# Kernel tuning notes

Measured on AMD Instinct MI355X. Metric: run time of the kernel, lower is better.

## Reference

```python
import jax, jax.numpy as jnp
import numpy as np

D = 64; T = 128; B = 64; R = 20; SEE = 10; H = 4; C = 4
N = 300000; P = 4000; K = 256


def setup_inputs() -> dict:
    key = jax.random.key(0)
    ks = jax.random.split(key, 24)
    g = lambda k, s: jax.random.normal(k, s, dtype=jnp.float32) * 0.05
    return {
        "prob_id": jax.random.randint(ks[0], (T, B), 0, P),
        "skills": jax.random.randint(ks[1], (T, B, C), 0, K),
        "response": jax.random.randint(ks[2], (T, B), 0, 2),
        "bg_index": jax.random.randint(ks[3], (T, B, R), 0, N),
        "mem_prob_ids": jax.random.randint(ks[4], (N,), 0, P),
        "mem_resp": jax.random.randint(ks[5], (N,), 0, 2),
        "mem_concepts": jax.random.randint(ks[6], (N, C), 0, K),
        "states_mem": g(ks[7], (N, D)),
        "concept_emb": g(ks[8], (K - 1, D)),
        "prob_emb": g(ks[9], (P - 1, D)),
        "W_pred": g(ks[10], (9 * D, 1)), "b_pred": jnp.zeros((1,), jnp.float32),
        "W_ih": g(ks[11], (4 * D, 3 * D)), "W_hh": g(ks[12], (D, 3 * D)),
        "b_ih": jnp.zeros((3 * D,), jnp.float32), "b_hh": jnp.zeros((3 * D,), jnp.float32),
        "W_batch": g(ks[13], (H, 3 * D, D)), "b_batch": jnp.zeros((H, D), jnp.float32),
        "W_bg": g(ks[14], (H, 3 * D, D)), "b_bg": jnp.zeros((H, D), jnp.float32),
        "W_bgint": g(ks[15], (6 * D, 6 * D)), "b_bgint": jnp.zeros((6 * D,), jnp.float32),
        "W_hisint": g(ks[16], (2 * D, 6 * D)), "b_hisint": jnp.zeros((6 * D,), jnp.float32),
        "W_inmap": g(ks[17], (10 * D, 4 * D)), "b_inmap": jnp.zeros((4 * D,), jnp.float32),
        "dir_w": g(ks[18], (2, 1)), "heads_map": g(ks[19], (H, 1)),
    }


def _forward(floats, ints):
    (states_mem, concept_emb, prob_emb, W_pred, b_pred, W_ih, W_hh, b_ih, b_hh,
     W_batch, b_batch, W_bg, b_bg, W_bgint, b_bgint, W_hisint, b_hisint,
     W_inmap, b_inmap, dir_w, heads_map) = floats
    prob_id, skills, response, bg_index, mem_prob_ids, mem_resp, mem_concepts = ints
    f32 = states_mem.dtype
    # embedding tables with zero row 0 (padding id)
    prob_cat = jnp.concatenate([jnp.zeros((1, D), f32), prob_emb], axis=0)
    conc_cat = jnp.concatenate([jnp.zeros((1, D), f32), concept_emb], axis=0)

    def prob_rep(pid, sk):
        pr = prob_cat[pid]                                     # [..., D]
        fsum = jnp.sum((sk != 0).astype(f32), axis=-1)
        div = jnp.where(fsum == 0, 1.0, fsum)[..., None]
        mean = jnp.sum(conc_cat[sk], axis=-2) / div            # masked-mean concept emb
        return jnp.concatenate([mean, pr], axis=-1)            # [..., 2D]

    dw = jax.nn.softmax(dir_w, axis=0)                          # [2,1]
    hm = heads_map[:, 0]                                        # [H]

    def step(carry, xt):
        h, h_buf, resp_buf, v_buf, t = carry
        pid, sk, resp, bgi = xt
        respf = resp.astype(f32)
        v = prob_rep(pid, sk)                                   # [B,2D]
        hidden_v = jnp.concatenate([h, v], axis=-1)             # [B,3D]
        bgi = bgi[:, :SEE]                                      # keep first see_ref refs
        bg_h = states_mem[bgi]                                  # [B,S,D] irregular gather
        bg_v = prob_rep(mem_prob_ids[bgi], mem_concepts[bgi])   # [B,S,2D]
        bg_r = mem_resp[bgi].astype(f32)[..., None]             # [B,S,1]
        all_hv = jnp.concatenate([bg_h, bg_v], axis=-1)         # [B,S,3D]
        bg_ctx = jnp.concatenate([all_hv * bg_r, all_hv * (1.0 - bg_r)], axis=-1)  # [B,S,6D]
        # multi-head attention over retrieved background states
        q = jnp.einsum('bk,hkd->bhd', hidden_v, W_batch) + b_batch[None]
        kk = jnp.einsum('bsk,hkd->bhsd', all_hv, W_bg) + b_bg[None, :, None, :]
        att = jax.nn.softmax(jnp.einsum('bhd,bhsd->bhs', q, kk) / np.sqrt(3.0 * D), axis=-1)
        heads = jnp.einsum('bhs,bsk->bhk', att, bg_ctx)          # [B,H,6D]
        bg_atts = jnp.einsum('bhk,h->bk', heads, hm)             # [B,6D]
        # attention over own history (positions 0..t valid)
        rb = resp_buf.astype(f32)[..., None]                     # [B,T+1,1]
        hr_cat = jnp.concatenate([h_buf * rb, h_buf * (1.0 - rb)], axis=-1)  # [B,T+1,2D]
        sc = jnp.einsum('bk,btk->bt', v, v_buf) / np.sqrt(2.0 * D)
        sc = jnp.where(jnp.arange(T + 1)[None, :] <= t, sc, -1e9)
        his_atts = jnp.einsum('bt,btk->bk', jax.nn.softmax(sc, axis=-1), hr_cat)  # [B,2D]
        peer = (bg_atts @ W_bgint + b_bgint) * dw[0, 0] + (his_atts @ W_hisint + b_hisint) * dw[1, 0]
        prob = (jnp.concatenate([peer, v, h], axis=-1) @ W_pred + b_pred)[:, 0]
        v_resp = jnp.concatenate([v * respf[:, None], v * (1.0 - respf[:, None])], axis=-1)
        gru_in = jnp.concatenate([peer, v_resp], axis=-1) @ W_inmap + b_inmap  # [B,4D]
        # GRU cell (torch GRUCell convention)
        gx = gru_in @ W_ih + b_ih
        gh = h @ W_hh + b_hh
        xr, xz, xn = jnp.split(gx, 3, axis=-1)
        hr, hz, hn = jnp.split(gh, 3, axis=-1)
        r = jax.nn.sigmoid(xr + hr)
        z = jax.nn.sigmoid(xz + hz)
        n = jnp.tanh(xn + r * hn)
        new_h = (1.0 - z) * n + z * h
        h_buf = h_buf.at[:, t + 1].set(new_h)
        resp_buf = resp_buf.at[:, t + 1].set(resp.astype(resp_buf.dtype))
        v_buf = v_buf.at[:, t + 1].set(v)
        return (new_h, h_buf, resp_buf, v_buf, t + 1), prob

    init = (jnp.zeros((B, D), f32), jnp.zeros((B, T + 1, D), f32),
            jnp.zeros((B, T + 1), jnp.int32), jnp.zeros((B, T + 1, 2 * D), f32),
            jnp.int32(0))
    xs = (prob_id, skills, response.astype(jnp.int32), bg_index)
    _, probs = jax.lax.scan(step, init, xs)                      # [T,B]
    return probs.T.reshape(-1)                                   # concat over batch, seq_num=T


def reference(prob_id, skills, response, bg_index, mem_prob_ids, mem_resp, mem_concepts,
              states_mem, concept_emb, prob_emb, W_pred, b_pred, W_ih, W_hh, b_ih, b_hh,
              W_batch, b_batch, W_bg, b_bg, W_bgint, b_bgint, W_hisint, b_hisint,
              W_inmap, b_inmap, dir_w, heads_map):
    floats = (states_mem, concept_emb, prob_emb, W_pred, b_pred, W_ih, W_hh, b_ih, b_hh,
              W_batch, b_batch, W_bg, b_bg, W_bgint, b_bgint, W_hisint, b_hisint,
              W_inmap, b_inmap, dir_w, heads_map)
    ints = (prob_id, skills, response, bg_index, mem_prob_ids, mem_resp, mem_concepts)
    return _forward(floats, ints)
```

## Files before the change

kernel.cpp:

```cpp
#include <hip/hip_runtime.h>
#include <hip/hip_bf16.h>

#define TT 128
#define BB 64
#define DD 64
#define RR 20
#define SEE 10
#define HH 4
#define CC 4
#define NITEM (TT*BB*SEE)
typedef __attribute__((ext_vector_type(8))) short short8;
typedef __attribute__((ext_vector_type(4))) float floatx4;

static __device__ __forceinline__ float wave_sum(float v) {
  v += __shfl_xor(v, 32); v += __shfl_xor(v, 16); v += __shfl_xor(v, 8);
  v += __shfl_xor(v, 4);  v += __shfl_xor(v, 2);  v += __shfl_xor(v, 1);
  return v;
}
static __device__ __forceinline__ float wave_max(float v) {
  v = fmaxf(v, __shfl_xor(v, 32)); v = fmaxf(v, __shfl_xor(v, 16)); v = fmaxf(v, __shfl_xor(v, 8));
  v = fmaxf(v, __shfl_xor(v, 4));  v = fmaxf(v, __shfl_xor(v, 2));  v = fmaxf(v, __shfl_xor(v, 1));
  return v;
}
static __device__ __forceinline__ unsigned short f2bf(float x) {
  __hip_bfloat16 h = __float2bfloat16(x);
  return *reinterpret_cast<unsigned short*>(&h);
}
static __device__ __forceinline__ unsigned int pack2(float lo, float hi) {
  return (unsigned int)f2bf(lo) | ((unsigned int)f2bf(hi) << 16);
}
static __device__ __forceinline__ void ldsbar() {
  asm volatile("s_waitcnt lgkmcnt(0)" ::: "memory");
  __builtin_amdgcn_s_barrier();
  asm volatile("" ::: "memory");
}

__global__ void build_v(const int* __restrict__ prob_id, const int* __restrict__ skills,
                        const float* __restrict__ concept_emb, const float* __restrict__ prob_emb,
                        float* __restrict__ V, float* __restrict__ VT) {
  int tb = blockIdx.x; int t = tb >> 6, b = tb & 63; int d = threadIdx.x;
  int pid = prob_id[tb];
  float pr = pid ? prob_emb[(pid - 1) * 64 + d] : 0.0f;
  int cnt = 0; float sum = 0.0f;
#pragma unroll
  for (int c = 0; c < 4; ++c) {
    int sk = skills[tb * 4 + c];
    if (sk) { ++cnt; sum += concept_emb[(sk - 1) * 64 + d]; }
  }
  float mean = sum / (float)(cnt ? cnt : 1);
  V[tb * 128 + d] = mean;
  V[tb * 128 + 64 + d] = pr;
  VT[b * 16384 + d * 128 + t] = mean;
  VT[b * 16384 + (64 + d) * 128 + t] = pr;
}

__global__ __launch_bounds__(256) void gemm_f32(
    const float* __restrict__ A, const float* __restrict__ B, float* __restrict__ C,
    const float* __restrict__ bias, int M, int N, int K,
    int lda, int ldb, int ldc, long sA, long sB, long sC, float scale) {
  __shared__ __align__(16) float As[64 * 36];
  __shared__ __align__(16) float Bs[32 * 64];
  const float* Ab = A + (long)blockIdx.z * sA;
  const float* Bb = B + (long)blockIdx.z * sB;
  float* Cb = C + (long)blockIdx.z * sC;
  int m0 = blockIdx.y * 64, n0 = blockIdx.x * 64;
  int tid = threadIdx.x;
  int ti = tid & 15, tj = tid >> 4;
  float acc[4][4] = {};
  for (int kc = 0; kc < K; kc += 32) {
#pragma unroll
    for (int p = 0; p < 2; ++p) {
      int q = tid + 256 * p;
      int row = q >> 3, kq = q & 7;
      *(float4*)&As[row * 36 + 4 * kq] = *(const float4*)&Ab[(size_t)(m0 + row) * lda + kc + 4 * kq];
    }
#pragma unroll
// ... 21 lines not shown
        }
      }
    }
    __syncthreads();
  }
  float4 bq = make_float4(0.f, 0.f, 0.f, 0.f);
  if (bias) bq = *(const float4*)&bias[n0 + 4 * tj];
#pragma unroll
  for (int m = 0; m < 4; ++m) {
    int row = m0 + ti + 16 * m;
    float4 o;
    o.x = acc[m][0] * scale + bq.x; o.y = acc[m][1] * scale + bq.y;
    o.z = acc[m][2] * scale + bq.z; o.w = acc[m][3] * scale + bq.w;
    *(float4*)&Cb[(size_t)row * ldc + n0 + 4 * tj] = o;
  }
}

__global__ __launch_bounds__(256) void k_small(
    const float* __restrict__ W_batch, const float* __restrict__ W_bg, const float* __restrict__ b_bg,
    const float* __restrict__ W_bgint, const float* __restrict__ b_bgint,
    const float* __restrict__ W_hisint, const float* __restrict__ b_hisint,
    const float* __restrict__ W_ih, const float* __restrict__ b_ih, const float* __restrict__ b_inmap,
    const float* __restrict__ W_pred, const float* __restrict__ b_pred, const float* __restrict__ dir_w,
    const float* __restrict__ M12, unsigned short* __restrict__ B1T, float* __restrict__ Hmix,
    float* __restrict__ WgT, float* __restrict__ WBvcat, float* __restrict__ Bgxv,
    float* __restrict__ c4, float* __restrict__ cgx, float* __restrict__ uh,
    float* __restrict__ bgp, float* __restrict__ c0, float* __restrict__ dwv) {
  int idx = blockIdx.x * 256 + threadIdx.x;
  const int R0 = 49152, R1 = 86016, R2 = 122880, R3 = 147456, R4 = 196608,
            R5 = 229376, R6 = 278528, R7 = 278784, R8 = 278976, R9 = 279104,
            R10 = 279488, R11 = 279489, R12 = 279491;
  if (idx < R0) {
    int k = idx >> 8, n = idx & 255; int h = n >> 6, i = n & 63;
    float s = 0.f;
    for (int d = 0; d < 64; ++d) s += W_bg[h * 12288 + k * 64 + d] * W_batch[h * 12288 + i * 64 + d];
    B1T[n * 192 + k] = f2bf(s);
  } else if (idx < R1) {
    int r = idx - R0; int k = r / 192, c = r - k * 192;
    float s = 0.f;
    for (int j = 0; j < 384; ++j) s += W_bgint[k * 384 + j] * M12[j * 192 + c];
    B1T[(256 + c) * 192 + k] = f2bf(s);
  } else if (idx < R2) {
    int r = idx - R1; int k = r / 192, c = r - k * 192;
    float s = 0.f;
    for (int j = 0; j < 384; ++j) s += W_bgint[(192 + k) * 384 + j] * M12[j * 192 + c];
    B1T[(448 + c) * 192 + k] = f2bf(s);
  } else if (idx < R3) {
    int r = idx - R2; int i = r / 192, c = r - i * 192;
    float s = 0.f;
    for (int j = 0; j < 384; ++j) s += W_hisint[i * 384 + j] * M12[j * 192 + c];
    Hmix[i * 192 + c] = s;
  } else if (idx < R4) {
    int r = idx - R3; int h = r / 12288; int rem = r - h * 12288; int d = rem / 192, k = rem - d * 192;
    WgT[r] = W_bg[h * 12288 + k * 64 + d];
  } else if (idx < R5) {
    int r = idx - R4; int i = r >> 8, n = r & 255; int h = n >> 6, d = n & 63;
    WBvcat[r] = W_batch[h * 12288 + (64 + i) * 64 + d];
  } else if (idx < R6) {
    int r = idx - R5; int i = r / 384, c = r - i * 384;
    Bgxv[r] = (c < 192) ? M12[(384 + i) * 192 + c] : M12[(512 + i) * 192 + (c - 192)];
  } else if (idx < R7) {
    int n = idx - R6; int h = n >> 6, i = n & 63;
    float s = 0.f;
    for (int d = 0; d < 64; ++d) s += W_batch[h * 12288 + i * 64 + d] * b_bg[h * 64 + d];
    c4[n] = s;
  } else if (idx < R8) {
    int c = idx - R7;
    float e0 = __expf(dir_w[0]), e1 = __expf(dir_w[1]);
    float dw0 = e0 / (e0 + e1), dw1 = e1 / (e0 + e1);
    float s = b_ih[c];
    for (int i = 0; i < 256; ++i) s += b_inmap[i] * W_ih[i * 192 + c];
    for (int k = 0; k < 384; ++k) s += (dw0 * b_bgint[k] + dw1 * b_hisint[k]) * M12[k * 192 + c];
    cgx[c] = s;
  } else if (idx < R9) {
    int i = idx - R8;
    float s = 0.f;
    for (int j = 0; j < 384; ++j) s += W_hisint[i * 384 + j] * W_pred[j];
    uh[i] = s;
  } else if (idx < R10) {
    int k = idx - R9;
    float s = 0.f;
    for (int j = 0; j < 384; ++j) s += W_bgint[k * 384 + j] * W_pred[j];
    bgp[k] = s;
  } else if (idx < R11) {
    float e0 = __expf(dir_w[0]), e1 = __expf(dir_w[1]);
    float dw0 = e0 / (e0 + e1), dw1 = e1 / (e0 + e1);
    float s = b_pred[0];
    for (int k = 0; k < 384; ++k) s += (dw0 * b_bgint[k] + dw1 * b_hisint[k]) * W_pred[k];
    c0[0] = s;
  } else if (idx < R12) {
    float e0 = __expf(dir_w[0]), e1 = __expf(dir_w[1]);
    dwv[idx - R11] = (idx == R11) ? e0 / (e0 + e1) : e1 / (e0 + e1);
  }
}

#define APAD 200
#define BPAD 40
__global__ __launch_bounds__(256) void big_gemm(
    const int* __restrict__ bg_index, const int* __restrict__ mem_prob_ids,
    const int* __restrict__ mem_resp, const int* __restrict__ mem_concepts,
    const float* __restrict__ states_mem, const float* __restrict__ concept_emb,
    const float* __restrict__ prob_emb, const unsigned short* __restrict__ B1T,
    const float* __restrict__ c4, float* __restrict__ P4s, float* __restrict__ Cg) {
  __shared__ unsigned short As[128 * APAD];
  __shared__ unsigned short Bs[128 * BPAD];
  __shared__ int bgi_l[128]; __shared__ int rf_l[128];
  int mt = blockIdx.x;
  int tid = threadIdx.x;
  int lane = tid & 63, wv = tid >> 6;
  if (tid < 128) {
    int item = mt * 128 + tid;
    int t = item / 640; int rem = item - t * 640; int b = rem / 10; int s = rem - b * 10;
    int g = bg_index[(t * 64 + b) * 20 + s];
    bgi_l[tid] = g;
    rf_l[tid] = mem_resp[g];
  }
  __syncthreads();
  {
    int half = lane >> 5;
    int hl = lane & 31;
    for (int rr = 0; rr < 32; rr += 2) {
      int r = wv * 32 + rr + half;
      int g = bgi_l[r];
      float2 sv = *(const float2*)&states_mem[g * 64 + 2 * hl];
      *(unsigned int*)&As[r * APAD + 2 * hl] = pack2(sv.x, sv.y);
      float s0 = 0.f, s1 = 0.f; int cnt = 0;
#pragma unroll
      for (int c = 0; c < 4; ++c) {
        int sk = mem_concepts[g * 4 + c];
        if (sk) { ++cnt; float2 e = *(const float2*)&concept_emb[(sk - 1) * 64 + 2 * hl]; s0 += e.x; s1 += e.y; }
      }
      float inv = 1.0f / (float)(cnt ? cnt : 1);
      *(unsigned int*)&As[r * APAD + 64 + 2 * hl] = pack2(s0 * inv, s1 * inv);
      int pid = mem_prob_ids[g];
      float2 pv = make_float2(0.f, 0.f);
      if (pid) pv = *(const float2*)&prob_emb[(pid - 1) * 64 + 2 * hl];
      *(unsigned int*)&As[r * APAD + 128 + 2 * hl] = pack2(pv.x, pv.y);
    }
  }
  int l15 = lane & 15, q = lane >> 4;
  int mh = (wv & 1) * 64, nh = (wv >> 1) * 64;
  const float invs192 = 0.07216878364870323f;
  for (int nt = 0; nt < 5; ++nt) {
    int n0 = nt * 128;
    floatx4 acc[4][4];
#pragma unroll
    for (int mi = 0; mi < 4; ++mi)
#pragma unroll
      for (int ni = 0; ni < 4; ++ni)
#pragma unroll
        for (int r = 0; r < 4; ++r) acc[mi][ni][r] = 0.f;
    for (int kc = 0; kc < 6; ++kc) {
      __syncthreads();
#pragma unroll
      for (int u = 0; u < 2; ++u) {
        int un = tid * 2 + u;
        int n = un >> 2, kk = (un & 3) * 8;
        *(float4*)&Bs[n * BPAD + kk] = *(const float4*)&B1T[(size_t)(n0 + n) * 192 + kc * 32 + kk];
      }
      __syncthreads();
      short8 a[4], bfr[4];
// ... 6 lines not shown
#pragma unroll
      for (int mi = 0; mi < 4; ++mi)
#pragma unroll
        for (int ni = 0; ni < 4; ++ni)
          acc[mi][ni] = __builtin_amdgcn_mfma_f32_16x16x32_bf16(a[mi], bfr[ni], acc[mi][ni], 0, 0, 0);
    }
    float c4v[4];
    if (n0 + nh < 256) {
#pragma unroll
      for (int ni = 0; ni < 4; ++ni) c4v[ni] = c4[n0 + nh + ni * 16 + l15];
    }
#pragma unroll
    for (int mi = 0; mi < 4; ++mi) {
#pragma unroll
      for (int r = 0; r < 4; ++r) {
        int row = mh + mi * 16 + q * 4 + r;
        int item = mt * 128 + row;
        int rf = rf_l[row];
#pragma unroll
        for (int ni = 0; ni < 4; ++ni) {
          int coln = n0 + nh + ni * 16 + l15;
          float o = acc[mi][ni][r];
          if (coln < 256) {
            P4s[(size_t)item * 256 + coln] = (o + c4v[ni]) * invs192;
          } else if (coln < 448) {
            if (rf) Cg[(size_t)item * 192 + (coln - 256)] = o;
          } else {
            if (!rf) Cg[(size_t)item * 192 + (coln - 448)] = o;
          }
        }
      }
    }
  }
}

__global__ __launch_bounds__(256) void k5(
    const int* __restrict__ bg_index, const int* __restrict__ mem_prob_ids,
    const int* __restrict__ mem_resp, const int* __restrict__ mem_concepts,
    const float* __restrict__ states_mem, const float* __restrict__ concept_emb,
    const float* __restrict__ prob_emb, const float* __restrict__ RQ, const float* __restrict__ QV,
    const float* __restrict__ b_bg, const float* __restrict__ bgp, const float* __restrict__ V,
    const float* __restrict__ W_pred, const float* __restrict__ c0,
    float* __restrict__ SQVb, float* __restrict__ cbp, float* __restrict__ PROBC) {
  int tb = blockIdx.x;
  int tid = threadIdx.x;
  int lane = tid & 63, wv = tid >> 6;
  __shared__ float ahv[10 * 196];
  __shared__ float rql[4 * 196];
  __shared__ float bgpl[384];
  __shared__ int bgi_l[10]; __shared__ int rf_s[10];
  __shared__ float cqb[4];
  if (tid < 10) { int g = bg_index[tb * 20 + tid]; bgi_l[tid] = g; rf_s[tid] = mem_resp[g]; }
  for (int i = tid; i < 384; i += 256) bgpl[i] = bgp[i];
  for (int i = tid; i < 768; i += 256) { int h = i / 192, c = i - h * 192; rql[h * 196 + c] = RQ[(size_t)tb * 768 + i]; }
  if (tid < 4) {
    float s = 0.f;
    for (int d = 0; d < 64; ++d) s += QV[tb * 256 + tid * 64 + d] * b_bg[tid * 64 + d];
    cqb[tid] = s;
  }
  __syncthreads();
  for (int s = 0; s < 10; ++s) {
    if (tid < 192) {
      int g = bgi_l[s]; float v;
      if (tid < 64) v = states_mem[g * 64 + tid];
      else if (tid < 128) {
        int d = tid - 64; float sum = 0.f; int cnt = 0;
#pragma unroll
        for (int c = 0; c < 4; ++c) { int sk = mem_concepts[g * 4 + c]; if (sk) { ++cnt; sum += concept_emb[(sk - 1) * 64 + d]; } }
        v = sum / (float)(cnt ? cnt : 1);
      } else {
        int pid = mem_prob_ids[g];
        v = pid ? prob_emb[(pid - 1) * 64 + (tid - 128)] : 0.0f;
      }
      ahv[s * 196 + tid] = v;
    }
  }
  __syncthreads();
  const float invs192 = 0.07216878364870323f;
  for (int q = 0; q < 10; ++q) {
    float v = ahv[q * 196 + lane] * rql[wv * 196 + lane]
            + ahv[q * 196 + 64 + lane] * rql[wv * 196 + 64 + lane]
            + ahv[q * 196 + 128 + lane] * rql[wv * 196 + 128 + lane];
    v = wave_sum(v);
    if (lane == 0) SQVb[tb * 40 + wv * 10 + q] = (v + cqb[wv]) * invs192;
  }
  if (wv == 0) {
    for (int q = 0; q < 10; ++q) {
      int off = rf_s[q] ? 0 : 192;
      float v = ahv[q * 196 + lane] * bgpl[off + lane]
              + ahv[q * 196 + 64 + lane] * bgpl[off + 64 + lane]
              + ahv[q * 196 + 128 + lane] * bgpl[off + 128 + lane];
      v = wave_sum(v);
      if (lane == 0) cbp[tb * 10 + q] = v;
    }
  }
  if (wv == 1) {
    float v = V[tb * 128 + lane] * W_pred[384 + lane] + V[tb * 128 + 64 + lane] * W_pred[448 + lane];
    v = wave_sum(v);
// ... 1 lines not shown
  }
}

__global__ __launch_bounds__(64) void prep_pw(const float* S, const int* response,
                                              float* PW, float* PR) {
  int bt = blockIdx.x; int b = bt >> 7, t = bt & 127;
  int lane = threadIdx.x;
  size_t row = (size_t)bt * 128;
  float s0 = (lane == 0) ? 0.f : ((lane <= t) ? S[row + lane - 1] : -1e30f);
  float s1 = (lane + 64 <= t) ? S[row + lane + 63] : -1e30f;
  float m = wave_max(fmaxf(s0, s1));
  float e0 = (lane <= t) ? __expf(s0 - m) : 0.f;
  float e1 = (lane + 64 <= t) ? __expf(s1 - m) : 0.f;
  float inv = 1.f / wave_sum(e0 + e1);
  float r0 = (lane >= 1) ? (float)response[(lane - 1) * 64 + b] : 0.f;
  float r1 = (float)response[(lane + 63) * 64 + b];
  PW[row + lane] = e0 * inv;
  PW[row + 64 + lane] = e1 * inv;
  PR[row + lane] = e0 * inv * r0;
  PR[row + 64 + lane] = e1 * inv * r1;
}

__global__ __launch_bounds__(512) void seq_kernel(
    const int* __restrict__ response, const float* __restrict__ P4s,
    const float* __restrict__ SQVb, const float* __restrict__ Cg,
    const float* __restrict__ GXV, const float* __restrict__ cbp,
    const float* __restrict__ PROBC, const float* __restrict__ PW,
    const float* __restrict__ PR, const float* __restrict__ Hmix,
    const float* __restrict__ W_hh, const float* __restrict__ b_hh,
    const float* __restrict__ cgx, const float* __restrict__ uh,
    const float* __restrict__ W_pred, const float* __restrict__ heads_map,
    const float* __restrict__ dwv, float* __restrict__ out) {
  int b = blockIdx.x;
  int tid = threadIdx.x;
  int lane = tid & 63, wv = tid >> 6;
  int cg3 = lane * 3;
  float hreg[16][3], wreg[8][3];
#pragma unroll
  for (int ii = 0; ii < 16; ++ii)
#pragma unroll
    for (int cc = 0; cc < 3; ++cc) hreg[ii][cc] = Hmix[(wv * 16 + ii) * 192 + cg3 + cc];
#pragma unroll
  for (int ii = 0; ii < 8; ++ii)
#pragma unroll
    for (int cc = 0; cc < 3; ++cc) wreg[ii][cc] = W_hh[(wv * 8 + ii) * 192 + cg3 + cc];
  float wph_reg[8], uh_reg[16];
  if (lane == 0) {
#pragma unroll
    for (int j = 0; j < 8; ++j) wph_reg[j] = W_pred[512 + wv * 8 + j];
#pragma unroll
    for (int ii = 0; ii < 16; ++ii) uh_reg[ii] = uh[wv * 16 + ii];
  }
  float bhh_reg = 0.f;
  if (tid >= 64 && tid < 256) bhh_reg = b_hh[tid - 64];
  float cgx0 = 0.f, cgx1 = 0.f, cgx2 = 0.f;
  if (tid < 64) { cgx0 = cgx[tid]; cgx1 = cgx[64 + tid]; cgx2 = cgx[128 + tid]; }
  float hmr = 0.f;
  if (tid >= 448 && tid < 452) hmr = heads_map[tid - 448];

  __shared__ __align__(16) float h_histT[64][132];
  __shared__ __align__(16) float PWl[128];
  __shared__ __align__(16) float PRl[128];
  __shared__ __align__(16) float h_cur[64];
  __shared__ __align__(16) float part_scT[40][12];
  __shared__ __align__(16) float e_l[40];
  __shared__ __align__(16) float inv_l[4];
  __shared__ __align__(16) float hisA[128];
  __shared__ __align__(16) float red8T[128][12];
  __shared__ float redWg[8][192];
  __shared__ float redWh[8][192];
  __shared__ float gh_l[192];
  __shared__ float hwp_p[8], phis_p[8];
  __shared__ int resp_l[128];

  if (tid < 64) { h_cur[tid] = 0.f; h_histT[tid][0] = 0.f; }
  if (tid >= 256 && tid < 384) resp_l[tid - 256] = response[(tid - 256) * 64 + b];
  float dw0 = dwv[0], dw1 = dwv[1];

  int sc_off = 0;
  if (lane < 40) { int hh = lane / 10, s = lane - hh * 10; sc_off = s * 256 + hh * 64 + wv * 8; }
  float4 pfa = make_float4(0, 0, 0, 0), pfb = pfa;
  if (lane < 40) {
    pfa = *(const float4*)&P4s[(size_t)b * 2560 + sc_off];
    pfb = *(const float4*)&P4s[(size_t)b * 2560 + sc_off + 4];
  }
  float pf_sqv = 0.f;
  if (tid >= 384 && tid < 424) pf_sqv = SQVb[b * 40 + (tid - 384)];
  float pf_cg0[10], pf_cg1[10], pf_cg2[10];
  float pf_gxA0 = 0.f, pf_gxA1 = 0.f, pf_gxA2 = 0.f, pf_gxB0 = 0.f, pf_gxB1 = 0.f, pf_gxB2 = 0.f;
  if (tid < 64) {
#pragma unroll
    for (int s = 0; s < 10; ++s) {
      size_t base = (size_t)(b * 10 + s) * 192;
      pf_cg0[s] = Cg[base + tid]; pf_cg1[s] = Cg[base + 64 + tid]; pf_cg2[s] = Cg[base + 128 + tid];
    }
    size_t gb = (size_t)b * 384;
    pf_gxA0 = GXV[gb + tid]; pf_gxA1 = GXV[gb + 64 + tid]; pf_gxA2 = GXV[gb + 128 + tid];
    pf_gxB0 = GXV[gb + 192 + tid]; pf_gxB1 = GXV[gb + 256 + tid]; pf_gxB2 = GXV[gb + 320 + tid];
  }
  float pf_cbp[10]; float pf_probc = 0.f;
  if (tid == 448) {
#pragma unroll
    for (int s = 0; s < 10; ++s) pf_cbp[s] = cbp[b * 10 + s];
    pf_probc = PROBC[b];
  }
  float4 pf_pw = make_float4(0, 0, 0, 0), pf_pr = pf_pw;
  if (tid >= 128 && tid < 160) pf_pw = *(const float4*)&PW[((size_t)(b * 128 + 0)) * 128 + 4 * (tid - 128)];
  else if (tid >= 160 && tid < 192) pf_pr = *(const float4*)&PR[((size_t)(b * 128 + 0)) * 128 + 4 * (tid - 160)];
  if (tid >= 128 && tid < 160) *(float4*)&PWl[4 * (tid - 128)] = pf_pw;
  else if (tid >= 160 && tid < 192) *(float4*)&PRl[4 * (tid - 160)] = pf_pr;
  if (tid >= 128 && tid < 160) pf_pw = *(const float4*)&PW[((size_t)(b * 128 + 1)) * 128 + 4 * (tid - 128)];
  else if (tid >= 160 && tid < 192) pf_pr = *(const float4*)&PR[((size_t)(b * 128 + 1)) * 128 + 4 * (tid - 160)];
  ldsbar();

  for (int t = 0; t < 128; ++t) {
    int tn = (t < 127) ? t + 1 : 127;
    int tbn = tn * 64 + b;
    float4 ha = *(const float4*)&h_cur[wv * 8];
    float4 hb = *(const float4*)&h_cur[wv * 8 + 4];
    if (lane < 40) {
      float v = ha.x * pfa.x + ha.y * pfa.y + ha.z * pfa.z + ha.w * pfa.w
              + hb.x * pfb.x + hb.y * pfb.y + hb.z * pfb.z + hb.w * pfb.w;
      part_scT[lane][wv] = v;
      pfa = *(const float4*)&P4s[(size_t)tbn * 2560 + sc_off];
      pfb = *(const float4*)&P4s[(size_t)tbn * 2560 + sc_off + 4];
    }
    {
      float hl[8] = {ha.x, ha.y, ha.z, ha.w, hb.x, hb.y, hb.z, hb.w};
      float l0 = 0.f, l1 = 0.f, l2 = 0.f;
#pragma unroll
      for (int ii = 0; ii < 8; ++ii) {
        l0 += hl[ii] * wreg[ii][0]; l1 += hl[ii] * wreg[ii][1]; l2 += hl[ii] * wreg[ii][2];
      }
      redWg[wv][cg3] = l0; redWg[wv][cg3 + 1] = l1; redWg[wv][cg3 + 2] = l2;
      if (lane == 0) {
        float hp = 0.f;
#pragma unroll
        for (int j = 0; j < 8; ++j) hp += hl[j] * wph_reg[j];
        hwp_p[wv] = hp;
      }
    }
    {
      int j0 = wv * 16;
      float aR = 0.f, aA = 0.f;
#pragma unroll
      for (int k = 0; k < 4; ++k) {
        float4 hv = *(const float4*)&h_histT[lane][j0 + 4 * k];
        float4 w4 = *(const float4*)&PWl[j0 + 4 * k];
        float4 r4 = *(const float4*)&PRl[j0 + 4 * k];
        aA += w4.x * hv.x + w4.y * hv.y + w4.z * hv.z + w4.w * hv.w;
        aR += r4.x * hv.x + r4.y * hv.y + r4.z * hv.z + r4.w * hv.w;
      }
      red8T[lane][wv] = aR; red8T[64 + lane][wv] = aA;
    }
    ldsbar();
    if (tid < 64) {
      float4 r0 = *(const float4*)&red8T[tid][0];
      float4 r1 = *(const float4*)&red8T[tid][4];
      float4 a0 = *(const float4*)&red8T[64 + tid][0];
      float4 a1 = *(const float4*)&red8T[64 + tid][4];
      float sR = r0.x + r0.y + r0.z + r0.w + r1.x + r1.y + r1.z + r1.w;
      float sA = a0.x + a0.y + a0.z + a0.w + a1.x + a1.y + a1.z + a1.w;
      hisA[tid] = sR; hisA[64 + tid] = sA - sR;
    } else if (tid < 256) {
      int c = tid - 64; float g = 0.f;
#pragma unroll
      for (int gg = 0; gg < 8; ++gg) g += redWg[gg][c];
      gh_l[c] = g + bhh_reg;
    } else if (tid >= 384 && tid < 424) {
      int p = tid - 384;
      float4 s0 = *(const float4*)&part_scT[p][0];
      float4 s1 = *(const float4*)&part_scT[p][4];
      float s = pf_sqv + s0.x + s0.y + s0.z + s0.w + s1.x + s1.y + s1.z + s1.w;
      e_l[p] = __expf(s);
      pf_sqv = SQVb[tbn * 40 + p];
    }
    ldsbar();
    {
      float4 h0 = *(const float4*)&hisA[wv * 16];
      float4 h1 = *(const float4*)&hisA[wv * 16 + 4];
      float4 h2 = *(const float4*)&hisA[wv * 16 + 8];
      float4 h3 = *(const float4*)&hisA[wv * 16 + 12];
      float hA[16] = {h0.x, h0.y, h0.z, h0.w, h1.x, h1.y, h1.z, h1.w,
                      h2.x, h2.y, h2.z, h2.w, h3.x, h3.y, h3.z, h3.w};
      float l0 = 0.f, l1 = 0.f, l2 = 0.f;
#pragma unroll
      for (int ii = 0; ii < 16; ++ii) {
        l0 += hA[ii] * hreg[ii][0]; l1 += hA[ii] * hreg[ii][1]; l2 += hA[ii] * hreg[ii][2];
      }
      redWh[wv][cg3] = l0; redWh[wv][cg3 + 1] = l1; redWh[wv][cg3 + 2] = l2;
      if (lane == 0) {
        float pp = 0.f;
#pragma unroll
        for (int ii = 0; ii < 16; ++ii) pp += hA[ii] * uh_reg[ii];
        phis_p[wv] = pp;
      }
// ... 16 lines not shown
      for (int s = 0; s < 10; ++s)
        ws[s] = iv.x * ev[s] + iv.y * ev[10 + s] + iv.z * ev[20 + s] + iv.w * ev[30 + s];
      if (tid < 64) {
        float gxh0 = 0.f, gxh1 = 0.f, gxh2 = 0.f;
#pragma unroll
        for (int g = 0; g < 8; ++g) {
          gxh0 += redWh[g][tid]; gxh1 += redWh[g][64 + tid]; gxh2 += redWh[g][128 + tid];
        }
        float gbg0 = 0.f, gbg1 = 0.f, gbg2 = 0.f;
#pragma unroll
        for (int s = 0; s < 10; ++s) {
          gbg0 += ws[s] * pf_cg0[s]; gbg1 += ws[s] * pf_cg1[s]; gbg2 += ws[s] * pf_cg2[s];
        }
        int rn = resp_l[t];
        float xr = dw0 * gbg0 + dw1 * gxh0 + (rn ? pf_gxA0 : pf_gxB0) + cgx0;
        float xz = dw0 * gbg1 + dw1 * gxh1 + (rn ? pf_gxA1 : pf_gxB1) + cgx1;
        float xn = dw0 * gbg2 + dw1 * gxh2 + (rn ? pf_gxA2 : pf_gxB2) + cgx2;
        float hr = gh_l[tid], hz = gh_l[64 + tid], hn = gh_l[128 + tid];
        float r = 1.f / (1.f + __expf(-(xr + hr)));
        float z = 1.f / (1.f + __expf(-(xz + hz)));
        float n = tanhf(xn + r * hn);
        float hnew = (1.f - z) * n + z * h_cur[tid];
        h_cur[tid] = hnew;
        if (t < 127) h_histT[tid][t + 1] = hnew;
#pragma unroll
        for (int s = 0; s < 10; ++s) {
          size_t base = (size_t)(tbn * 10 + s) * 192;
          pf_cg0[s] = Cg[base + tid]; pf_cg1[s] = Cg[base + 64 + tid]; pf_cg2[s] = Cg[base + 128 + tid];
        }
        size_t gb = (size_t)tbn * 384;
        pf_gxA0 = GXV[gb + tid]; pf_gxA1 = GXV[gb + 64 + tid]; pf_gxA2 = GXV[gb + 128 + tid];
        pf_gxB0 = GXV[gb + 192 + tid]; pf_gxB1 = GXV[gb + 256 + tid]; pf_gxB2 = GXV[gb + 320 + tid];
      } else {
        float pbg = 0.f;
#pragma unroll
        for (int s = 0; s < 10; ++s) pbg += ws[s] * pf_cbp[s];
        float ph = 0.f, hw = 0.f;
#pragma unroll
        for (int g = 0; g < 8; ++g) { ph += phis_p[g]; hw += hwp_p[g]; }
        out[b * 128 + t] = dw0 * pbg + dw1 * ph + hw + pf_probc;
#pragma unroll
        for (int s = 0; s < 10; ++s) pf_cbp[s] = cbp[tbn * 10 + s];
        pf_probc = PROBC[tbn];
      }
    } else if (tid >= 128 && tid < 192) {
      if (tid < 160) *(float4*)&PWl[4 * (tid - 128)] = pf_pw;
      else *(float4*)&PRl[4 * (tid - 160)] = pf_pr;
      int rn2 = (t + 2 < 128) ? t + 2 : 127;
      if (tid < 160) pf_pw = *(const float4*)&PW[((size_t)(b * 128 + rn2)) * 128 + 4 * (tid - 128)];
      else pf_pr = *(const float4*)&PR[((size_t)(b * 128 + rn2)) * 128 + 4 * (tid - 160)];
    }
    ldsbar();
  }
}

// ... 17 lines not shown
  const float* b_ih     = (const float*)d_in[14];
  const float* b_hh     = (const float*)d_in[15];
  const float* W_batch  = (const float*)d_in[16];
  const float* b_batch  = (const float*)d_in[17];
  const float* W_bg     = (const float*)d_in[18];
  const float* b_bg     = (const float*)d_in[19];
  const float* W_bgint  = (const float*)d_in[20];
  const float* b_bgint  = (const float*)d_in[21];
  const float* W_hisint = (const float*)d_in[22];
  const float* b_hisint = (const float*)d_in[23];
  const float* W_inmap  = (const float*)d_in[24];
  const float* b_inmap  = (const float*)d_in[25];
  const float* dir_w    = (const float*)d_in[26];
  const float* heads_map= (const float*)d_in[27];
  float* out = (float*)d_out;

  float* w = (float*)d_ws;
  size_t off = 0;
  auto alloc = [&](size_t n) { float* p = w + off; off += (n + 3) & ~(size_t)3; return p; };
  float* M12    = alloc(640 * 192);
  unsigned short* B1T = (unsigned short*)alloc(640 * 192 / 2);
  float* Hmix   = alloc(128 * 192);
  float* WgT    = alloc(4 * 192 * 64);
  float* WBvcat = alloc(128 * 256);
  float* Bgxv   = alloc(128 * 384);
  float* c4     = alloc(256);
  float* cgx    = alloc(192);
  float* uh     = alloc(128);
  float* bgp    = alloc(384);
  float* c0     = alloc(1);
  float* dwv    = alloc(2);
  float* V      = alloc((size_t)8192 * 128);
  float* VT     = alloc((size_t)64 * 128 * 128);
  float* QV     = alloc((size_t)8192 * 256);
  float* RQ     = alloc((size_t)8192 * 768);
  float* GXV    = alloc((size_t)8192 * 384);
  float* S      = alloc((size_t)64 * 128 * 128);
  float* PR     = alloc((size_t)64 * 128 * 128);
  float* P4s    = alloc((size_t)NITEM * 256);
  float* Cg     = alloc((size_t)NITEM * 192);
  float* SQVb   = alloc((size_t)8192 * 40);
  float* cbp    = alloc((size_t)NITEM);
  float* PROBC  = alloc(8192);
  (void)ws_size; (void)in_sizes; (void)n_in; (void)out_size;

  build_v<<<8192, 64, 0, stream>>>(prob_id, skills, concept_emb, prob_emb, V, VT);
  gemm_f32<<<dim3(3, 10, 1), 256, 0, stream>>>(W_inmap, W_ih, M12, nullptr,
      640, 192, 256, 256, 192, 192, 0, 0, 0, 1.0f);
  k_small<<<1092, 256, 0, stream>>>(W_batch, W_bg, b_bg, W_bgint, b_bgint, W_hisint, b_hisint,
      W_ih, b_ih, b_inmap, W_pred, b_pred, dir_w, M12, B1T, Hmix, WgT, WBvcat, Bgxv,
      c4, cgx, uh, bgp, c0, dwv);
  gemm_f32<<<dim3(4, 128, 1), 256, 0, stream>>>(V, WBvcat, QV, b_batch,
      8192, 256, 128, 128, 256, 256, 0, 0, 0, 1.0f);
  gemm_f32<<<dim3(3, 128, 4), 256, 0, stream>>>(QV, WgT, RQ, nullptr,
      8192, 192, 64, 256, 192, 768, 64, 12288, 192, 1.0f);
  gemm_f32<<<dim3(6, 128, 1), 256, 0, stream>>>(V, Bgxv, GXV, nullptr,
      8192, 384, 128, 128, 384, 384, 0, 0, 0, 1.0f);
  gemm_f32<<<dim3(2, 2, 64), 256, 0, stream>>>(V, VT, S, nullptr,
      128, 128, 128, 8192, 128, 128, 128, 16384, 16384, 0.08838834764831845f);
  prep_pw<<<8192, 64, 0, stream>>>(S, response, S, PR);
  big_gemm<<<dim3(640), 256, 0, stream>>>(bg_index, mem_prob_ids, mem_resp, mem_concepts,
      states_mem, concept_emb, prob_emb, B1T, c4, P4s, Cg);
  k5<<<8192, 256, 0, stream>>>(bg_index, mem_prob_ids, mem_resp, mem_concepts,
      states_mem, concept_emb, prob_emb, RQ, QV, b_bg, bgp, V, W_pred, c0, SQVb, cbp, PROBC);
  seq_kernel<<<64, 512, 0, stream>>>(response, P4s, SQVb, Cg, GXV, cbp, PROBC,
      S, PR, Hmix, W_hh, b_hh, cgx, uh, W_pred, heads_map, dwv, out);
}
```

Baseline: 840.7 us.

## Precompute bf16 history gather once, merge QV/GXV GEMMs, store P4s in bf16

```diff
diff --git a/kernel.cpp b/kernel.cpp
--- a/kernel.cpp
+++ b/kernel.cpp
@@ -3,12 +3,8 @@
 
 #define TT 128
 #define BB 64
-#define DD 64
-#define RR 20
+#define NITEM (TT*BB*SEE)
 #define SEE 10
-#define HH 4
-#define CC 4
-#define NITEM (TT*BB*SEE)
 typedef __attribute__((ext_vector_type(8))) short short8;
 typedef __attribute__((ext_vector_type(4))) float floatx4;
 
@@ -25,6 +21,10 @@
 static __device__ __forceinline__ unsigned short f2bf(float x) {
   __hip_bfloat16 h = __float2bfloat16(x);
   return *reinterpret_cast<unsigned short*>(&h);
+}
+static __device__ __forceinline__ float bf2f(unsigned short u) {
+  unsigned v = ((unsigned)u) << 16;
+  return __builtin_bit_cast(float, v);
 }
 static __device__ __forceinline__ unsigned int pack2(float lo, float hi) {
   return (unsigned int)f2bf(lo) | ((unsigned int)f2bf(hi) << 16);
@@ -52,6 +52,36 @@
   V[tb * 128 + 64 + d] = pr;
   VT[b * 16384 + d * 128 + t] = mean;
   VT[b * 16384 + (64 + d) * 128 + t] = pr;
+}
+
+__global__ __launch_bounds__(256) void gather_ahv(
+    const int* __restrict__ bg_index, const int* __restrict__ mem_prob_ids,
+    const int* __restrict__ mem_concepts, const float* __restrict__ states_mem,
+    const float* __restrict__ concept_emb, const float* __restrict__ prob_emb,
+    unsigned short* __restrict__ AHV) {
+  int gid = blockIdx.x * 256 + threadIdx.x;
+  int item = gid / 96, c2 = gid - 96 * item; int d = 2 * c2;
+  int t = item / 640; int rem = item - t * 640; int b = rem / 10; int s = rem - b * 10;
+  int g = bg_index[(t * 64 + b) * 20 + s];
+  float v0, v1;
+  if (d < 64) {
+    float2 sv = *(const float2*)&states_mem[g * 64 + d];
+    v0 = sv.x; v1 = sv.y;
+  } else if (d < 128) {
+    int dd = d - 64; float s0 = 0.f, s1 = 0.f; int cnt = 0;
+#pragma unroll
+    for (int c = 0; c < 4; ++c) {
+      int sk = mem_concepts[g * 4 + c];
+      if (sk) { ++cnt; float2 e = *(const float2*)&concept_emb[(sk - 1) * 64 + dd]; s0 += e.x; s1 += e.y; }
+    }
+    float inv = 1.0f / (float)(cnt ? cnt : 1);
+    v0 = s0 * inv; v1 = s1 * inv;
+  } else {
+    int dd = d - 128; int pid = mem_prob_ids[g];
+    if (pid) { float2 pv = *(const float2*)&prob_emb[(pid - 1) * 64 + dd]; v0 = pv.x; v1 = pv.y; }
+    else { v0 = 0.f; v1 = 0.f; }
+  }
+  *(unsigned int*)&AHV[(size_t)item * 192 + d] = pack2(v0, v1);
 }
 
 __global__ __launch_bounds__(256) void gemm_f32(
@@ -119,14 +149,15 @@
     const float* __restrict__ W_hisint, const float* __restrict__ b_hisint,
     const float* __restrict__ W_ih, const float* __restrict__ b_ih, const float* __restrict__ b_inmap,
     const float* __restrict__ W_pred, const float* __restrict__ b_pred, const float* __restrict__ dir_w,
+    const float* __restrict__ b_batch,
     const float* __restrict__ M12, unsigned short* __restrict__ B1T, float* __restrict__ Hmix,
-    float* __restrict__ WgT, float* __restrict__ WBvcat, float* __restrict__ Bgxv,
+    float* __restrict__ WgT, float* __restrict__ BQG, float* __restrict__ biasQG,
     float* __restrict__ c4, float* __restrict__ cgx, float* __restrict__ uh,
     float* __restrict__ bgp, float* __restrict__ c0, float* __restrict__ dwv) {
   int idx = blockIdx.x * 256 + threadIdx.x;
   const int R0 = 49152, R1 = 86016, R2 = 122880, R3 = 147456, R4 = 196608,
             R5 = 229376, R6 = 278528, R7 = 278784, R8 = 278976, R9 = 279104,
-            R10 = 279488, R11 = 279489, R12 = 279491;
+            R10 = 279488, R11 = 279489, R12 = 279491, R13 = 280131;
   if (idx < R0) {
     int k = idx >> 8, n = idx & 255; int h = n >> 6, i = n & 63;
     float s = 0.f;
@@ -152,10 +183,10 @@
     WgT[r] = W_bg[h * 12288 + k * 64 + d];
   } else if (idx < R5) {
     int r = idx - R4; int i = r >> 8, n = r & 255; int h = n >> 6, d = n & 63;
-    WBvcat[r] = W_batch[h * 12288 + (64 + i) * 64 + d];
+    BQG[i * 640 + n] = W_batch[h * 12288 + (64 + i) * 64 + d];
   } else if (idx < R6) {
     int r = idx - R5; int i = r / 384, c = r - i * 384;
-    Bgxv[r] = (c < 192) ? M12[(384 + i) * 192 + c] : M12[(512 + i) * 192 + (c - 192)];
+    BQG[i * 640 + 256 + c] = (c < 192) ? M12[(384 + i) * 192 + c] : M12[(512 + i) * 192 + (c - 192)];
   } else if (idx < R7) {
     int n = idx - R6; int h = n >> 6, i = n & 63;
     float s = 0.f;
@@ -188,20 +219,21 @@
   } else if (idx < R12) {
     float e0 = __expf(dir_w[0]), e1 = __expf(dir_w[1]);
     dwv[idx - R11] = (idx == R11) ? e0 / (e0 + e1) : e1 / (e0 + e1);
+  } else if (idx < R13) {
+    int i = idx - R12;
+    biasQG[i] = (i < 256) ? b_batch[i] : 0.f;
   }
 }
 
 #define APAD 200
 #define BPAD 40
 __global__ __launch_bounds__(256) void big_gemm(
-    const int* __restrict__ bg_index, const int* __restrict__ mem_prob_ids,
-    const int* __restrict__ mem_resp, const int* __restrict__ mem_concepts,
-    const float* __restrict__ states_mem, const float* __restrict__ concept_emb,
-    const float* __restrict__ prob_emb, const unsigned short* __restrict__ B1T,
-    const float* __restrict__ c4, float* __restrict__ P4s, float* __restrict__ Cg) {
+    const int* __restrict__ bg_index, const int* __restrict__ mem_resp,
+    const unsigned short* __restrict__ AHV, const unsigned short* __restrict__ B1T,
+    const float* __restrict__ c4, unsigned short* __restrict__ P4s16, float* __restrict__ Cg) {
   __shared__ unsigned short As[128 * APAD];
   __shared__ unsigned short Bs[128 * BPAD];
-  __shared__ int bgi_l[128]; __shared__ int rf_l[128];
+  __shared__ int rf_l[128];
   int mt = blockIdx.x;
   int tid = threadIdx.x;
   int lane = tid & 63, wv = tid >> 6;
@@ -209,31 +241,11 @@
     int item = mt * 128 + tid;
     int t = item / 640; int rem = item - t * 640; int b = rem / 10; int s = rem - b * 10;
     int g = bg_index[(t * 64 + b) * 20 + s];
-    bgi_l[tid] = g;
     rf_l[tid] = mem_resp[g];
   }
-  __syncthreads();
-  {
-    int half = lane >> 5;
-    int hl = lane & 31;
-    for (int rr = 0; rr < 32; rr += 2) {
-      int r = wv * 32 + rr + half;
-      int g = bgi_l[r];
-      float2 sv = *(const float2*)&states_mem[g * 64 + 2 * hl];
-      *(unsigned int*)&As[r * APAD + 2 * hl] = pack2(sv.x, sv.y);
-      float s0 = 0.f, s1 = 0.f; int cnt = 0;
-#pragma unroll
-      for (int c = 0; c < 4; ++c) {
-        int sk = mem_concepts[g * 4 + c];
-        if (sk) { ++cnt; float2 e = *(const float2*)&concept_emb[(sk - 1) * 64 + 2 * hl]; s0 += e.x; s1 += e.y; }
-      }
-      float inv = 1.0f / (float)(cnt ? cnt : 1);
-      *(unsigned int*)&As[r * APAD + 64 + 2 * hl] = pack2(s0 * inv, s1 * inv);
-      int pid = mem_prob_ids[g];
-      float2 pv = make_float2(0.f, 0.f);
-      if (pid) pv = *(const float2*)&prob_emb[(pid - 1) * 64 + 2 * hl];
-      *(unsigned int*)&As[r * APAD + 128 + 2 * hl] = pack2(pv.x, pv.y);
-    }
+  for (int i = tid; i < 128 * 24; i += 256) {
+    int row = i / 24, c = i - 24 * row;
+    *(float4*)&As[row * APAD + c * 8] = *(const float4*)&AHV[(size_t)(mt * 128 + row) * 192 + c * 8];
   }
   int l15 = lane & 15, q = lane >> 4;
   int mh = (wv & 1) * 64, nh = (wv >> 1) * 64;
@@ -286,7 +298,7 @@
           int coln = n0 + nh + ni * 16 + l15;
           float o = acc[mi][ni][r];
           if (coln < 256) {
-            P4s[(size_t)item * 256 + coln] = (o + c4v[ni]) * invs192;
+            P4s16[(size_t)item * 256 + coln] = f2bf((o + c4v[ni]) * invs192);
           } else if (coln < 448) {
             if (rf) Cg[(size_t)item * 192 + (coln - 256)] = o;
           } else {
@@ -299,11 +311,10 @@
 }
 
 __global__ __launch_bounds__(256) void k5(
-    const int* __restrict__ bg_index, const int* __restrict__ mem_prob_ids,
-    const int* __restrict__ mem_resp, const int* __restrict__ mem_concepts,
-    const float* __restrict__ states_mem, const float* __restrict__ concept_emb,
-    const float* __restrict__ prob_emb, const float* __restrict__ RQ, const float* __restrict__ QV,
-    const float* __restrict__ b_bg, const float* __restrict__ bgp, const float* __restrict__ V,
+    const int* __restrict__ bg_index, const int* __restrict__ mem_resp,
+    const unsigned short* __restrict__ AHV, const float* __restrict__ RQ,
+    const float* __restrict__ QVG, const float* __restrict__ b_bg,
+    const float* __restrict__ bgp, const float* __restrict__ V,
     const float* __restrict__ W_pred, const float* __restrict__ c0,
     float* __restrict__ SQVb, float* __restrict__ cbp, float* __restrict__ PROBC) {
   int tb = blockIdx.x;
@@ -312,32 +323,22 @@
   __shared__ float ahv[10 * 196];
   __shared__ float rql[4 * 196];
   __shared__ float bgpl[384];
-  __shared__ int bgi_l[10]; __shared__ int rf_s[10];
+  __shared__ int rf_s[10];
   __shared__ float cqb[4];
-  if (tid < 10) { int g = bg_index[tb * 20 + tid]; bgi_l[tid] = g; rf_s[tid] = mem_resp[g]; }
+  if (tid < 10) { int g = bg_index[tb * 20 + tid]; rf_s[tid] = mem_resp[g]; }
   for (int i = tid; i < 384; i += 256) bgpl[i] = bgp[i];
   for (int i = tid; i < 768; i += 256) { int h = i / 192, c = i - h * 192; rql[h * 196 + c] = RQ[(size_t)tb * 768 + i]; }
+  {
+    const unsigned short* AH = &AHV[(size_t)tb * 10 * 192];
+    for (int i = tid; i < 1920; i += 256) {
+      int s = i / 192, c = i - 192 * s;
+      ahv[s * 196 + c] = bf2f(AH[s * 192 + c]);
+    }
+  }
   if (tid < 4) {
     float s = 0.f;
-    for (int d = 0; d < 64; ++d) s += QV[tb * 256 + tid * 64 + d] * b_bg[tid * 64 + d];
+    for (int d = 0; d < 64; ++d) s += QVG[(size_t)tb * 640 + tid * 64 + d] * b_bg[tid * 64 + d];
     cqb[tid] = s;
-  }
-  __syncthreads();
-  for (int s = 0; s < 10; ++s) {
-    if (tid < 192) {
-      int g = bgi_l[s]; float v;
-      if (tid < 64) v = states_mem[g * 64 + tid];
-      else if (tid < 128) {
-        int d = tid - 64; float sum = 0.f; int cnt = 0;
-#pragma unroll
-        for (int c = 0; c < 4; ++c) { int sk = mem_concepts[g * 4 + c]; if (sk) { ++cnt; sum += concept_emb[(sk - 1) * 64 + d]; } }
-        v = sum / (float)(cnt ? cnt : 1);
-      } else {
-        int pid = mem_prob_ids[g];
-        v = pid ? prob_emb[(pid - 1) * 64 + (tid - 128)] : 0.0f;
-      }
-      ahv[s * 196 + tid] = v;
-    }
   }
   __syncthreads();
   const float invs192 = 0.07216878364870323f;
@@ -385,9 +386,9 @@
 }
 
 __global__ __launch_bounds__(512) void seq_kernel(
-    const int* __restrict__ response, const float* __restrict__ P4s,
+    const int* __restrict__ response, const unsigned short* __restrict__ P4s16,
     const float* __restrict__ SQVb, const float* __restrict__ Cg,
-    const float* __restrict__ GXV, const float* __restrict__ cbp,
+    const float* __restrict__ QVG, const float* __restrict__ cbp,
     const float* __restrict__ PROBC, const float* __restrict__ PW,
     const float* __restrict__ PR, const float* __restrict__ Hmix,
     const float* __restrict__ W_hh, const float* __restrict__ b_hh,
@@ -421,32 +422,30 @@
   float hmr = 0.f;
   if (tid >= 448 && tid < 452) hmr = heads_map[tid - 448];
 
-  __shared__ __align__(16) float h_histT[64][132];
+  __shared__ float h_hist[128][64];
   __shared__ __align__(16) float PWl[128];
   __shared__ __align__(16) float PRl[128];
   __shared__ __align__(16) float h_cur[64];
-  __shared__ __align__(16) float part_scT[40][12];
+  __shared__ float part_sc[8][40];
   __shared__ __align__(16) float e_l[40];
   __shared__ __align__(16) float inv_l[4];
   __shared__ __align__(16) float hisA[128];
-  __shared__ __align__(16) float red8T[128][12];
+  __shared__ float red8[8][128];
   __shared__ float redWg[8][192];
   __shared__ float redWh[8][192];
   __shared__ float gh_l[192];
   __shared__ float hwp_p[8], phis_p[8];
   __shared__ int resp_l[128];
 
-  if (tid < 64) { h_cur[tid] = 0.f; h_histT[tid][0] = 0.f; }
+  for (int i = tid; i < 128 * 64; i += 512) ((float*)h_hist)[i] = 0.f;
+  if (tid < 64) h_cur[tid] = 0.f;
   if (tid >= 256 && tid < 384) resp_l[tid - 256] = response[(tid - 256) * 64 + b];
   float dw0 = dwv[0], dw1 = dwv[1];
 
   int sc_off = 0;
   if (lane < 40) { int hh = lane / 10, s = lane - hh * 10; sc_off = s * 256 + hh * 64 + wv * 8; }
-  float4 pfa = make_float4(0, 0, 0, 0), pfb = pfa;
-  if (lane < 40) {
-    pfa = *(const float4*)&P4s[(size_t)b * 2560 + sc_off];
-    pfb = *(const float4*)&P4s[(size_t)b * 2560 + sc_off + 4];
-  }
+  short8 pf8 = {};
+  if (lane < 40) pf8 = *(const short8*)&P4s16[(size_t)b * 2560 + sc_off];
   float pf_sqv = 0.f;
   if (tid >= 384 && tid < 424) pf_sqv = SQVb[b * 40 + (tid - 384)];
   float pf_cg0[10], pf_cg1[10], pf_cg2[10];
@@ -457,9 +456,9 @@
       size_t base = (size_t)(b * 10 + s) * 192;
       pf_cg0[s] = Cg[base + tid]; pf_cg1[s] = Cg[base + 64 + tid]; pf_cg2[s] = Cg[base + 128 + tid];
     }
-    size_t gb = (size_t)b * 384;
-    pf_gxA0 = GXV[gb + tid]; pf_gxA1 = GXV[gb + 64 + tid]; pf_gxA2 = GXV[gb + 128 + tid];
-    pf_gxB0 = GXV[gb + 192 + tid]; pf_gxB1 = GXV[gb + 256 + tid]; pf_gxB2 = GXV[gb + 320 + tid];
+    size_t gb = (size_t)b * 640 + 256;
+    pf_gxA0 = QVG[gb + tid]; pf_gxA1 = QVG[gb + 64 + tid]; pf_gxA2 = QVG[gb + 128 + tid];
+    pf_gxB0 = QVG[gb + 192 + tid]; pf_gxB1 = QVG[gb + 256 + tid]; pf_gxB2 = QVG[gb + 320 + tid];
   }
   float pf_cbp[10]; float pf_probc = 0.f;
   if (tid == 448) {
@@ -482,11 +481,11 @@
     float4 ha = *(const float4*)&h_cur[wv * 8];
     float4 hb = *(const float4*)&h_cur[wv * 8 + 4];
     if (lane < 40) {
-      float v = ha.x * pfa.x + ha.y * pfa.y + ha.z * pfa.z + ha.w * pfa.w
-              + hb.x * pfb.x + hb.y * pfb.y + hb.z * pfb.z + hb.w * pfb.w;
-      part_scT[lane][wv] = v;
-      pfa = *(const float4*)&P4s[(size_t)tbn * 2560 + sc_off];
-      pfb = *(const float4*)&P4s[(size_t)tbn * 2560 + sc_off + 4];
+      const unsigned short* pp = (const unsigned short*)&pf8;
+      float v = ha.x * bf2f(pp[0]) + ha.y * bf2f(pp[1]) + ha.z * bf2f(pp[2]) + ha.w * bf2f(pp[3])
+              + hb.x * bf2f(pp[4]) + hb.y * bf2f(pp[5]) + hb.z * bf2f(pp[6]) + hb.w * bf2f(pp[7]);
+      part_sc[wv][lane] = v;
+      pf8 = *(const short8*)&P4s16[(size_t)tbn * 2560 + sc_off];
     }
     {
       float hl[8] = {ha.x, ha.y, ha.z, ha.w, hb.x, hb.y, hb.z, hb.w};
@@ -507,23 +506,17 @@
       int j0 = wv * 16;
       float aR = 0.f, aA = 0.f;
 #pragma unroll
-      for (int k = 0; k < 4; ++k) {
-        float4 hv = *(const float4*)&h_histT[lane][j0 + 4 * k];
-        float4 w4 = *(const float4*)&PWl[j0 + 4 * k];
-        float4 r4 = *(const float4*)&PRl[j0 + 4 * k];
-        aA += w4.x * hv.x + w4.y * hv.y + w4.z * hv.z + w4.w * hv.w;
-        aR += r4.x * hv.x + r4.y * hv.y + r4.z * hv.z + r4.w * hv.w;
-      }
-      red8T[lane][wv] = aR; red8T[64 + lane][wv] = aA;
+      for (int k = 0; k < 16; ++k) {
+        float hv = h_hist[j0 + k][lane];
+        aA += PWl[j0 + k] * hv; aR += PRl[j0 + k] * hv;
+      }
+      red8[wv][lane] = aR; red8[wv][64 + lane] = aA;
     }
     ldsbar();
     if (tid < 64) {
-      float4 r0 = *(const float4*)&red8T[tid][0];
-      float4 r1 = *(const float4*)&red8T[tid][4];
-      float4 a0 = *(const float4*)&red8T[64 + tid][0];
-      float4 a1 = *(const float4*)&red8T[64 + tid][4];
-      float sR = r0.x + r0.y + r0.z + r0.w + r1.x + r1.y + r1.z + r1.w;
-      float sA = a0.x + a0.y + a0.z + a0.w + a1.x + a1.y + a1.z + a1.w;
+      float sR = 0.f, sA = 0.f;
+#pragma unroll
+      for (int g = 0; g < 8; ++g) { sR += red8[g][tid]; sA += red8[g][64 + tid]; }
       hisA[tid] = sR; hisA[64 + tid] = sA - sR;
     } else if (tid < 256) {
       int c = tid - 64; float g = 0.f;
@@ -532,9 +525,9 @@
       gh_l[c] = g + bhh_reg;
     } else if (tid >= 384 && tid < 424) {
       int p = tid - 384;
-      float4 s0 = *(const float4*)&part_scT[p][0];
-      float4 s1 = *(const float4*)&part_scT[p][4];
-      float s = pf_sqv + s0.x + s0.y + s0.z + s0.w + s1.x + s1.y + s1.z + s1.w;
+      float s = pf_sqv;
+#pragma unroll
+      for (int w = 0; w < 8; ++w) s += part_sc[w][p];
       e_l[p] = __expf(s);
       pf_sqv = SQVb[tbn * 40 + p];
     }
@@ -597,15 +590,15 @@
         float n = tanhf(xn + r * hn);
         float hnew = (1.f - z) * n + z * h_cur[tid];
         h_cur[tid] = hnew;
-        if (t < 127) h_histT[tid][t + 1] = hnew;
+        if (t < 127) h_hist[t + 1][tid] = hnew;
 #pragma unroll
         for (int s = 0; s < 10; ++s) {
           size_t base = (size_t)(tbn * 10 + s) * 192;
           pf_cg0[s] = Cg[base + tid]; pf_cg1[s] = Cg[base + 64 + tid]; pf_cg2[s] = Cg[base + 128 + tid];
         }
-        size_t gb = (size_t)tbn * 384;
-        pf_gxA0 = GXV[gb + tid]; pf_gxA1 = GXV[gb + 64 + tid]; pf_gxA2 = GXV[gb + 128 + tid];
-        pf_gxB0 = GXV[gb + 192 + tid]; pf_gxB1 = GXV[gb + 256 + tid]; pf_gxB2 = GXV[gb + 320 + tid];
+        size_t gb = (size_t)tbn * 640 + 256;
+        pf_gxA0 = QVG[gb + tid]; pf_gxA1 = QVG[gb + 64 + tid]; pf_gxA2 = QVG[gb + 128 + tid];
+        pf_gxB0 = QVG[gb + 192 + tid]; pf_gxB1 = QVG[gb + 256 + tid]; pf_gxB2 = QVG[gb + 320 + tid];
       } else {
         float pbg = 0.f;
 #pragma unroll
@@ -669,8 +662,8 @@
   unsigned short* B1T = (unsigned short*)alloc(640 * 192 / 2);
   float* Hmix   = alloc(128 * 192);
   float* WgT    = alloc(4 * 192 * 64);
-  float* WBvcat = alloc(128 * 256);
-  float* Bgxv   = alloc(128 * 384);
+  float* BQG    = alloc(128 * 640);
+  float* biasQG = alloc(640);
   float* c4     = alloc(256);
   float* cgx    = alloc(192);
   float* uh     = alloc(128);
@@ -679,12 +672,12 @@
   float* dwv    = alloc(2);
   float* V      = alloc((size_t)8192 * 128);
   float* VT     = alloc((size_t)64 * 128 * 128);
-  float* QV     = alloc((size_t)8192 * 256);
+  float* QVG    = alloc((size_t)8192 * 640);
   float* RQ     = alloc((size_t)8192 * 768);
-  float* GXV    = alloc((size_t)8192 * 384);
   float* S      = alloc((size_t)64 * 128 * 128);
   float* PR     = alloc((size_t)64 * 128 * 128);
-  float* P4s    = alloc((size_t)NITEM * 256);
+  unsigned short* AHV = (unsigned short*)alloc((size_t)NITEM * 192 / 2);
+  unsigned short* P4s16 = (unsigned short*)alloc((size_t)NITEM * 256 / 2);
   float* Cg     = alloc((size_t)NITEM * 192);
   float* SQVb   = alloc((size_t)8192 * 40);
   float* cbp    = alloc((size_t)NITEM);
@@ -692,24 +685,23 @@
   (void)ws_size; (void)in_sizes; (void)n_in; (void)out_size;
 
   build_v<<<8192, 64, 0, stream>>>(prob_id, skills, concept_emb, prob_emb, V, VT);
+  gather_ahv<<<NITEM * 96 / 256, 256, 0, stream>>>(bg_index, mem_prob_ids, mem_concepts,
+      states_mem, concept_emb, prob_emb, AHV);
   gemm_f32<<<dim3(3, 10, 1), 256, 0, stream>>>(W_inmap, W_ih, M12, nullptr,
       640, 192, 256, 256, 192, 192, 0, 0, 0, 1.0f);
-  k_small<<<1092, 256, 0, stream>>>(W_batch, W_bg, b_bg, W_bgint, b_bgint, W_hisint, b_hisint,
-      W_ih, b_ih, b_inmap, W_pred, b_pred, dir_w, M12, B1T, Hmix, WgT, WBvcat, Bgxv,
+  k_small<<<1095, 256, 0, stream>>>(W_batch, W_bg, b_bg, W_bgint, b_bgint, W_hisint, b_hisint,
+      W_ih, b_ih, b_inmap, W_pred, b_pred, dir_w, b_batch, M12, B1T, Hmix, WgT, BQG, biasQG,
       c4, cgx, uh, bgp, c0, dwv);
-  gemm_f32<<<dim3(4, 128, 1), 256, 0, stream>>>(V, WBvcat, QV, b_batch,
-      8192, 256, 128, 128, 256, 256, 0, 0, 0, 1.0f);
-  gemm_f32<<<dim3(3, 128, 4), 256, 0, stream>>>(QV, WgT, RQ, nullptr,
-      8192, 192, 64, 256, 192, 768, 64, 12288, 192, 1.0f);
-  gemm_f32<<<dim3(6, 128, 1), 256, 0, stream>>>(V, Bgxv, GXV, nullptr,
-      8192, 384, 128, 128, 384, 384, 0, 0, 0, 1.0f);
+  gemm_f32<<<dim3(10, 128, 1), 256, 0, stream>>>(V, BQG, QVG, biasQG,
+      8192, 640, 128, 128, 640, 640, 0, 0, 0, 1.0f);
+  gemm_f32<<<dim3(3, 128, 4), 256, 0, stream>>>(QVG, WgT, RQ, nullptr,
+      8192, 192, 64, 640, 192, 768, 64, 12288, 192, 1.0f);
   gemm_f32<<<dim3(2, 2, 64), 256, 0, stream>>>(V, VT, S, nullptr,
       128, 128, 128, 8192, 128, 128, 128, 16384, 16384, 0.08838834764831845f);
   prep_pw<<<8192, 64, 0, stream>>>(S, response, S, PR);
-  big_gemm<<<dim3(640), 256, 0, stream>>>(bg_index, mem_prob_ids, mem_resp, mem_concepts,
-      states_mem, concept_emb, prob_emb, B1T, c4, P4s, Cg);
-  k5<<<8192, 256, 0, stream>>>(bg_index, mem_prob_ids, mem_resp, mem_concepts,
-      states_mem, concept_emb, prob_emb, RQ, QV, b_bg, bgp, V, W_pred, c0, SQVb, cbp, PROBC);
-  seq_kernel<<<64, 512, 0, stream>>>(response, P4s, SQVb, Cg, GXV, cbp, PROBC,
+  big_gemm<<<dim3(640), 256, 0, stream>>>(bg_index, mem_resp, AHV, B1T, c4, P4s16, Cg);
+  k5<<<8192, 256, 0, stream>>>(bg_index, mem_resp, AHV, RQ, QVG, b_bg, bgp, V, W_pred, c0,
+      SQVb, cbp, PROBC);
+  seq_kernel<<<64, 512, 0, stream>>>(response, P4s16, SQVb, Cg, QVG, cbp, PROBC,
       S, PR, Hmix, W_hh, b_hh, cgx, uh, W_pred, heads_map, dwv, out);
 }
```

After: 762.9 us. -9.3%, faster.
